# Optimization experiments

Measured on AMD Instinct MI355X. Metric: run time of the kernel, lower is better.

Reference implementation:

```python
import jax, jax.numpy as jnp
import numpy as np

N_NODES, N_EDGES, D = 50000, 640000, 128

def setup_inputs() -> dict:
    key = jax.random.key(0)
    ks = jax.random.split(key, 8)
    s = 0.05
    return {
        'node_h': jax.random.normal(ks[0], (N_NODES, D), jnp.float32),
        'edge_h': jax.random.normal(ks[1], (N_EDGES, D), jnp.float32),
        'src': jax.random.randint(ks[2], (N_EDGES,), 0, N_NODES, jnp.int32),
        'dst': jax.random.randint(ks[3], (N_EDGES,), 0, N_NODES, jnp.int32),
        'We1': jax.random.normal(ks[4], (3 * D, D), jnp.float32) * s,
        'be1': jnp.zeros((D,), jnp.float32),
        'We2': jax.random.normal(ks[5], (D, D), jnp.float32) * s,
        'be2': jnp.zeros((D,), jnp.float32),
        'Wn1': jax.random.normal(ks[6], (2 * D, D), jnp.float32) * s,
        'bn1': jnp.zeros((D,), jnp.float32),
        'Wn2': jax.random.normal(ks[7], (D, D), jnp.float32) * s,
        'bn2': jnp.zeros((D,), jnp.float32),
    }

def reference(node_h, edge_h, src, dst, We1, be1, We2, be2, Wn1, bn1, Wn2, bn2):
    # edge update: concat(src h, dst h, edge h) -> edge MLP  [E, 3D] -> [E, D]
    e_in = jnp.concatenate([node_h[src], node_h[dst], edge_h], axis=-1)
    e_new = jax.nn.relu(e_in @ We1 + be1) @ We2 + be2
    # message = copy_e('h'), reduce = sum -> segment_sum over destination nodes
    agg_m = jax.ops.segment_sum(e_new, dst, num_segments=node_h.shape[0])
    # node update: concat(agg_m, node h) -> node MLP  [N, 2D] -> [N, D]
    n_in = jnp.concatenate([agg_m, node_h], axis=-1)
    n_new = jax.nn.relu(n_in @ Wn1 + bn1) @ Wn2 + bn2
    return n_new
```

## Files before the change

### kernel.cpp

```cpp
#include <hip/hip_runtime.h>

#define NN 50000
#define NE 640000
#define DD 128

typedef float f32x4 __attribute__((ext_vector_type(4)));
typedef __bf16 bf16x8 __attribute__((ext_vector_type(8)));
typedef unsigned short u16x8 __attribute__((ext_vector_type(8)));

__device__ inline __bf16 f2bf(float f) {
  unsigned u = __builtin_bit_cast(unsigned, f);
  u = (u + 0x7fffu + ((u >> 16) & 1u)) >> 16;
  unsigned short h = (unsigned short)u;
  return __builtin_bit_cast(__bf16, h);
}
__device__ inline unsigned short f2bfu(float f) {
  return __builtin_bit_cast(unsigned short, f2bf(f));
}
__device__ inline float bf2f(unsigned bits16) {
  return __builtin_bit_cast(float, bits16 << 16);
}
__device__ inline float bfval(__bf16 h) {
  return bf2f((unsigned)__builtin_bit_cast(unsigned short, h));
}

__device__ inline bf16x8 load8(const float* __restrict__ p) {
  f32x4 a = *(const f32x4*)p;
  f32x4 b = *(const f32x4*)(p + 4);
  bf16x8 o;
  o[0] = f2bf(a[0]); o[1] = f2bf(a[1]); o[2] = f2bf(a[2]); o[3] = f2bf(a[3]);
  o[4] = f2bf(b[0]); o[5] = f2bf(b[1]); o[6] = f2bf(b[2]); o[7] = f2bf(b[3]);
  return o;
}

#define MFMA16(a, b, c) __builtin_amdgcn_mfma_f32_16x16x32_bf16((a), (b), (c), 0, 0, 0)

__global__ void prep_kernel(const float* __restrict__ We1, const float* __restrict__ We2,
                            const float* __restrict__ Wn1, const float* __restrict__ Wn2,
                            __bf16* __restrict__ We1t, __bf16* __restrict__ We2t,
                            __bf16* __restrict__ Wn1t, __bf16* __restrict__ Wn2t) {
  int i = blockIdx.x * blockDim.x + threadIdx.x;
  if (i < 49152) {
    int n = i / 384, k = i % 384;
    We1t[i] = f2bf(We1[k * 128 + n]);
  } else if (i < 65536) {
    int j = i - 49152; int n = j / 128, k = j % 128;
    We2t[j] = f2bf(We2[k * 128 + n]);
  } else if (i < 98304) {
    int j = i - 65536; int n = j / 256, k = j % 256;
    Wn1t[j] = f2bf(Wn1[k * 128 + n]);
  } else if (i < 114688) {
    int j = i - 98304; int n = j / 128, k = j % 128;
    Wn2t[j] = f2bf(Wn2[k * 128 + n]);
  }
}

__global__ void conv_node_kernel(const float* __restrict__ nh,
                                 unsigned short* __restrict__ nhb) {
  int i = blockIdx.x * 256 + threadIdx.x;
  if (i >= NN * DD / 8) return;
  const float* p = nh + (size_t)i * 8;
  f32x4 a = *(const f32x4*)p;
  f32x4 b = *(const f32x4*)(p + 4);
  u16x8 o;
  o[0] = f2bfu(a[0]); o[1] = f2bfu(a[1]); o[2] = f2bfu(a[2]); o[3] = f2bfu(a[3]);
  o[4] = f2bfu(b[0]); o[5] = f2bfu(b[1]); o[6] = f2bfu(b[2]); o[7] = f2bfu(b[3]);
  *(u16x8*)(nhb + (size_t)i * 8) = o;
}

__global__ void hist_kernel(const int* __restrict__ dst, int* __restrict__ counts) {
  int i = blockIdx.x * 256 + threadIdx.x;
  if (i < NE) atomicAdd(&counts[dst[i]], 1);
}
__global__ void scan1_kernel(const int* __restrict__ counts, int* __restrict__ basearr,
                             int* __restrict__ partials) {
  __shared__ int sd[256];
  int t = threadIdx.x;
  int i = blockIdx.x * 256 + t;
  int v = (i < NN) ? counts[i] : 0;
  sd[t] = v; __syncthreads();
  for (int off = 1; off < 256; off <<= 1) {
    int x = (t >= off) ? sd[t - off] : 0;
    __syncthreads();
    sd[t] += x;
    __syncthreads();
  }
  if (i < NN) basearr[i] = sd[t] - v;
  if (t == 255) partials[blockIdx.x] = sd[255];
}
__global__ void scan2_kernel(const int* __restrict__ partials, int* __restrict__ poff,
                             int nparts) {
  __shared__ int sd[256];
  int t = threadIdx.x;
  int v = (t < nparts) ? partials[t] : 0;
  sd[t] = v; __syncthreads();
  for (int off = 1; off < 256; off <<= 1) {
    int x = (t >= off) ? sd[t - off] : 0;
    __syncthreads();
    sd[t] += x;
    __syncthreads();
  }
  if (t < nparts) poff[t] = sd[t] - v;
}
__global__ void scan3_kernel(int* __restrict__ basearr, const int* __restrict__ poff) {
  int i = blockIdx.x * 256 + threadIdx.x;
  if (i < NN) basearr[i] += poff[blockIdx.x];
}
__global__ void scatter_kernel(const int* __restrict__ src, const int* __restrict__ dst,
                               const int* __restrict__ basearr, int* __restrict__ cursor,
                               int* __restrict__ eids, int* __restrict__ sidv,
                               int* __restrict__ dstv) {
  int i = blockIdx.x * 256 + threadIdx.x;
  if (i < NE) {
    int d = dst[i];
    int p = basearr[d] + atomicAdd(&cursor[d], 1);
    eids[p] = i;
    sidv[p] = src[i];
    dstv[p] = d;
  }
}

__global__ __launch_bounds__(256) void edge_agg_kernel(
    const unsigned short* __restrict__ nhb, const float* __restrict__ edge_h,
    const int* __restrict__ eids, const int* __restrict__ sidv,
    const int* __restrict__ dstv,
    const __bf16* __restrict__ We1t, const float* __restrict__ be1,
    float* __restrict__ S) {
  __shared__ unsigned short h1[128 * 136];
  __shared__ int dloc[128];
  const int tid = (int)threadIdx.x;
  const int w = tid >> 6;
  const int l = tid & 63;
  const int lm = l & 15;
  const int q = l >> 4;
  const int e0 = (int)blockIdx.x * 128;
  const int row0 = w * 32;

  if (tid < 128) dloc[tid] = dstv[e0 + tid];

  const int p0 = e0 + row0 + lm;
  const int p1 = p0 + 16;
  const unsigned short* gA0[2] = {nhb + (size_t)sidv[p0] * DD, nhb + (size_t)dstv[p0] * DD};
  const unsigned short* gA1[2] = {nhb + (size_t)sidv[p1] * DD, nhb + (size_t)dstv[p1] * DD};
  const float* eh0 = edge_h + (size_t)eids[p0] * DD;
  const float* eh1 = edge_h + (size_t)eids[p1] * DD;

  f32x4 acc[2][8];
#pragma unroll
  for (int nt = 0; nt < 8; ++nt) {
    float b = be1[nt * 16 + lm];
    acc[0][nt] = (f32x4){b, b, b, b};
    acc[1][nt] = (f32x4){b, b, b, b};
  }

#pragma unroll
  for (int step = 0; step < 8; ++step) {
    const int region = step >> 2;
    const int col = ((step & 3) * 32) + q * 8;
    bf16x8 a0 = __builtin_bit_cast(bf16x8, *(const u16x8*)(gA0[region] + col));
    bf16x8 a1 = __builtin_bit_cast(bf16x8, *(const u16x8*)(gA1[region] + col));
    const __bf16* bp = We1t + (size_t)lm * 384 + step * 32 + q * 8;
#pragma unroll
    for (int nt = 0; nt < 8; ++nt) {
      bf16x8 bb = *(const bf16x8*)(bp + nt * 16 * 384);
      acc[0][nt] = MFMA16(a0, bb, acc[0][nt]);
      acc[1][nt] = MFMA16(a1, bb, acc[1][nt]);
    }
  }
#pragma unroll
  for (int s2 = 0; s2 < 4; ++s2) {
    const int col = s2 * 32 + q * 8;
    bf16x8 a0 = load8(eh0 + col);
    bf16x8 a1 = load8(eh1 + col);
    const __bf16* bp = We1t + (size_t)lm * 384 + (8 + s2) * 32 + q * 8;
#pragma unroll
    for (int nt = 0; nt < 8; ++nt) {
      bf16x8 bb = *(const bf16x8*)(bp + nt * 16 * 384);
      acc[0][nt] = MFMA16(a0, bb, acc[0][nt]);
      acc[1][nt] = MFMA16(a1, bb, acc[1][nt]);
    }
  }

#pragma unroll
  for (int t = 0; t < 2; ++t)
#pragma unroll
    for (int nt = 0; nt < 8; ++nt)
#pragma unroll
      for (int r = 0; r < 4; ++r) {
        float v = acc[t][nt][r];
        v = v > 0.f ? v : 0.f;
        int m = row0 + t * 16 + q * 4 + r;
        h1[m * 136 + nt * 16 + lm] = f2bfu(v);
      }
  __syncthreads();

  {
    const int col = tid & 127;
    const int rbeg = (tid >> 7) * 64;
    const int rend = rbeg + 64;
    float a = 0.f;
    int dcur = dloc[rbeg];
    for (int r = rbeg; r < rend; ++r) {
      int d = dloc[r];
      if (d != dcur) {
        unsafeAtomicAdd(&S[(size_t)dcur * DD + col], a);
        a = 0.f;
        dcur = d;
      }
      a += bf2f((unsigned)h1[r * 136 + col]);
    }
    unsafeAtomicAdd(&S[(size_t)dcur * DD + col], a);
  }
}

__global__ __launch_bounds__(256) void node_kernel2(
    const unsigned short* __restrict__ nhb, const float* __restrict__ S,
    const int* __restrict__ counts,
    const __bf16* __restrict__ We2t, const float* __restrict__ be2,
    const __bf16* __restrict__ Wn1t, const float* __restrict__ bn1,
    const __bf16* __restrict__ Wn2t, const float* __restrict__ bn2,
    float* __restrict__ out) {
  __shared__ unsigned short h1[128 * 136];
  const int tid = (int)threadIdx.x;
  const int w = tid >> 6;
  const int l = tid & 63;
  const int lm = l & 15;
  const int q = l >> 4;
  const int n0 = (int)blockIdx.x * 128;
  const int row0 = w * 32;

  int r0 = n0 + row0 + lm;
  int r1 = r0 + 16;
  int c0 = r0 < NN ? r0 : NN - 1;
  int c1 = r1 < NN ? r1 : NN - 1;
  const float* s0p = S + (size_t)c0 * DD;
  const float* s1p = S + (size_t)c1 * DD;

  f32x4 acc[2][8];

  {
    float cnt0[4], cnt1[4];
#pragma unroll
    for (int r = 0; r < 4; ++r) {
      int ra = n0 + row0 + q * 4 + r;
      int rb = ra + 16;
      cnt0[r] = (ra < NN) ? (float)counts[ra] : 0.f;
      cnt1[r] = (rb < NN) ? (float)counts[rb] : 0.f;
    }
#pragma unroll
    for (int nt = 0; nt < 8; ++nt) {
      float b = be2[nt * 16 + lm];
#pragma unroll
      for (int r = 0; r < 4; ++r) {
        acc[0][nt][r] = cnt0[r] * b;
        acc[1][nt][r] = cnt1[r] * b;
      }
    }
  }
#pragma unroll
  for (int step = 0; step < 4; ++step) {
    const int col = step * 32 + q * 8;
    f32x4 x0a = *(const f32x4*)(s0p + col);
    f32x4 x0b = *(const f32x4*)(s0p + col + 4);
    f32x4 x1a = *(const f32x4*)(s1p + col);
    f32x4 x1b = *(const f32x4*)(s1p + col + 4);
    bf16x8 h0, l0, h8, l8;
#pragma unroll
    for (int j = 0; j < 4; ++j) {
      float v = x0a[j]; __bf16 hh = f2bf(v);
      h0[j] = hh; l0[j] = f2bf(v - bfval(hh));
      v = x0b[j]; hh = f2bf(v);
      h0[j + 4] = hh; l0[j + 4] = f2bf(v - bfval(hh));
      v = x1a[j]; hh = f2bf(v);
      h8[j] = hh; l8[j] = f2bf(v - bfval(hh));
      v = x1b[j]; hh = f2bf(v);
      h8[j + 4] = hh; l8[j + 4] = f2bf(v - bfval(hh));
    }
    const __bf16* bp = We2t + (size_t)lm * 128 + step * 32 + q * 8;
#pragma unroll
    for (int nt = 0; nt < 8; ++nt) {
      bf16x8 bb = *(const bf16x8*)(bp + nt * 16 * 128);
      acc[0][nt] = MFMA16(h0, bb, acc[0][nt]);
      acc[0][nt] = MFMA16(l0, bb, acc[0][nt]);
      acc[1][nt] = MFMA16(h8, bb, acc[1][nt]);
      acc[1][nt] = MFMA16(l8, bb, acc[1][nt]);
    }
  }

#pragma unroll
  for (int t = 0; t < 2; ++t)
#pragma unroll
    for (int nt = 0; nt < 8; ++nt)
#pragma unroll
      for (int r = 0; r < 4; ++r) {
        int m = row0 + t * 16 + q * 4 + r;
        h1[m * 136 + nt * 16 + lm] = f2bfu(acc[t][nt][r]);
      }
  __syncthreads();

#pragma unroll
  for (int nt = 0; nt < 8; ++nt) {
    float b = bn1[nt * 16 + lm];
    acc[0][nt] = (f32x4){b, b, b, b};
    acc[1][nt] = (f32x4){b, b, b, b};
  }
#pragma unroll
  for (int step = 0; step < 8; ++step) {
    bf16x8 a0, a1;
    if (step < 4) {
      a0 = __builtin_bit_cast(bf16x8, *(const u16x8*)&h1[(row0 + lm) * 136 + step * 32 + q * 8]);
      a1 = __builtin_bit_cast(bf16x8, *(const u16x8*)&h1[(row0 + 16 + lm) * 136 + step * 32 + q * 8]);
    } else {
      const int col = (step - 4) * 32 + q * 8;
      a0 = __builtin_bit_cast(bf16x8, *(const u16x8*)(nhb + (size_t)c0 * DD + col));
      a1 = __builtin_bit_cast(bf16x8, *(const u16x8*)(nhb + (size_t)c1 * DD + col));
    }
    const __bf16* bp = Wn1t + (size_t)lm * 256 + step * 32 + q * 8;
#pragma unroll
    for (int nt = 0; nt < 8; ++nt) {
      bf16x8 bb = *(const bf16x8*)(bp + nt * 16 * 256);
      acc[0][nt] = MFMA16(a0, bb, acc[0][nt]);
      acc[1][nt] = MFMA16(a1, bb, acc[1][nt]);
    }
  }
  __syncthreads();

#pragma unroll
  for (int t = 0; t < 2; ++t)
#pragma unroll
    for (int nt = 0; nt < 8; ++nt)
#pragma unroll
      for (int r = 0; r < 4; ++r) {
        float v = acc[t][nt][r];
        v = v > 0.f ? v : 0.f;
        int m = row0 + t * 16 + q * 4 + r;
        h1[m * 136 + nt * 16 + lm] = f2bfu(v);
      }
  __syncthreads();

#pragma unroll
  for (int nt = 0; nt < 8; ++nt) {
    float b = bn2[nt * 16 + lm];
    acc[0][nt] = (f32x4){b, b, b, b};
    acc[1][nt] = (f32x4){b, b, b, b};
  }
#pragma unroll
  for (int step = 0; step < 4; ++step) {
    bf16x8 a0 = __builtin_bit_cast(bf16x8, *(const u16x8*)&h1[(row0 + lm) * 136 + step * 32 + q * 8]);
    bf16x8 a1 = __builtin_bit_cast(bf16x8, *(const u16x8*)&h1[(row0 + 16 + lm) * 136 + step * 32 + q * 8]);
    const __bf16* bp = Wn2t + (size_t)lm * 128 + step * 32 + q * 8;
#pragma unroll
    for (int nt = 0; nt < 8; ++nt) {
      bf16x8 bb = *(const bf16x8*)(bp + nt * 16 * 128);
      acc[0][nt] = MFMA16(a0, bb, acc[0][nt]);
      acc[1][nt] = MFMA16(a1, bb, acc[1][nt]);
    }
  }

#pragma unroll
  for (int t = 0; t < 2; ++t) {
#pragma unroll
    for (int r = 0; r < 4; ++r) {
      int node = n0 + row0 + t * 16 + q * 4 + r;
      if (node < NN) {
        float* orow = out + (size_t)node * DD + lm;
#pragma unroll
        for (int nt = 0; nt < 8; ++nt)
          orow[nt * 16] = acc[t][nt][r];
      }
    }
  }
}

__global__ __launch_bounds__(256) void edge_fb_kernel(
    const float* __restrict__ node_h, const float* __restrict__ edge_h,
    const int* __restrict__ src, const int* __restrict__ dst,
    const __bf16* __restrict__ We1t, const float* __restrict__ be1,
    const __bf16* __restrict__ We2t, const float* __restrict__ be2,
    float* __restrict__ agg) {
  __shared__ unsigned short h1[128 * 136];
  const int tid = (int)threadIdx.x;
  const int w = tid >> 6;
  const int l = tid & 63;
  const int lm = l & 15;
  const int q = l >> 4;
  const int e0 = (int)blockIdx.x * 128;
  const int row0 = w * 32;

  const int eA0 = e0 + row0 + lm;
  const int eA1 = eA0 + 16;
  const float* srcA0[3];
  const float* srcA1[3];
  srcA0[0] = node_h + (size_t)src[eA0] * DD;
  srcA0[1] = node_h + (size_t)dst[eA0] * DD;
  srcA0[2] = edge_h + (size_t)eA0 * DD;
  srcA1[0] = node_h + (size_t)src[eA1] * DD;
  srcA1[1] = node_h + (size_t)dst[eA1] * DD;
  srcA1[2] = edge_h + (size_t)eA1 * DD;

  f32x4 acc[2][8];
#pragma unroll
  for (int nt = 0; nt < 8; ++nt) {
    float b = be1[nt * 16 + lm];
    acc[0][nt] = (f32x4){b, b, b, b};
    acc[1][nt] = (f32x4){b, b, b, b};
  }
#pragma unroll
  for (int step = 0; step < 12; ++step) {
    const int region = step >> 2;
    const int col = ((step & 3) * 32) + q * 8;
    bf16x8 a0 = load8(srcA0[region] + col);
    bf16x8 a1 = load8(srcA1[region] + col);
    const __bf16* bp = We1t + (size_t)lm * 384 + step * 32 + q * 8;
#pragma unroll
    for (int nt = 0; nt < 8; ++nt) {
      bf16x8 bb = *(const bf16x8*)(bp + nt * 16 * 384);
      acc[0][nt] = MFMA16(a0, bb, acc[0][nt]);
      acc[1][nt] = MFMA16(a1, bb, acc[1][nt]);
    }
  }
#pragma unroll
  for (int t = 0; t < 2; ++t)
#pragma unroll
    for (int nt = 0; nt < 8; ++nt)
#pragma unroll
      for (int r = 0; r < 4; ++r) {
        float v = acc[t][nt][r];
        v = v > 0.f ? v : 0.f;
        int m = row0 + t * 16 + q * 4 + r;
        h1[m * 136 + nt * 16 + lm] = f2bfu(v);
      }
  __syncthreads();
#pragma unroll
  for (int nt = 0; nt < 8; ++nt) {
    float b = be2[nt * 16 + lm];
    acc[0][nt] = (f32x4){b, b, b, b};
    acc[1][nt] = (f32x4){b, b, b, b};
  }
#pragma unroll
  for (int step = 0; step < 4; ++step) {
    bf16x8 a0 = __builtin_bit_cast(bf16x8, *(const u16x8*)&h1[(row0 + lm) * 136 + step * 32 + q * 8]);
    bf16x8 a1 = __builtin_bit_cast(bf16x8, *(const u16x8*)&h1[(row0 + 16 + lm) * 136 + step * 32 + q * 8]);
    const __bf16* bp = We2t + (size_t)lm * 128 + step * 32 + q * 8;
#pragma unroll
    for (int nt = 0; nt < 8; ++nt) {
      bf16x8 bb = *(const bf16x8*)(bp + nt * 16 * 128);
      acc[0][nt] = MFMA16(a0, bb, acc[0][nt]);
      acc[1][nt] = MFMA16(a1, bb, acc[1][nt]);
    }
  }
#pragma unroll
  for (int t = 0; t < 2; ++t) {
#pragma unroll
    for (int r = 0; r < 4; ++r) {
      int e = e0 + row0 + t * 16 + q * 4 + r;
      float* arow = agg + (size_t)dst[e] * DD + lm;
#pragma unroll
      for (int nt = 0; nt < 8; ++nt)
        unsafeAtomicAdd(arow + nt * 16, acc[t][nt][r]);
    }
  }
}

__global__ __launch_bounds__(256) void node_fb_kernel(
    const float* __restrict__ node_h, const float* __restrict__ agg,
    const __bf16* __restrict__ Wn1t, const float* __restrict__ bn1,
    const __bf16* __restrict__ Wn2t, const float* __restrict__ bn2,
    float* __restrict__ out) {
  __shared__ unsigned short h1[128 * 136];
  const int tid = (int)threadIdx.x;
  const int w = tid >> 6;
  const int l = tid & 63;
  const int lm = l & 15;
  const int q = l >> 4;
  const int n0 = (int)blockIdx.x * 128;
  const int row0 = w * 32;

  int r0 = n0 + row0 + lm;
  int r1 = r0 + 16;
  int c0 = r0 < NN ? r0 : NN - 1;
  int c1 = r1 < NN ? r1 : NN - 1;
  const float* srcA0[2] = {agg + (size_t)c0 * DD, node_h + (size_t)c0 * DD};
  const float* srcA1[2] = {agg + (size_t)c1 * DD, node_h + (size_t)c1 * DD};

  f32x4 acc[2][8];
#pragma unroll
  for (int nt = 0; nt < 8; ++nt) {
    float b = bn1[nt * 16 + lm];
    acc[0][nt] = (f32x4){b, b, b, b};
    acc[1][nt] = (f32x4){b, b, b, b};
  }
#pragma unroll
  for (int step = 0; step < 8; ++step) {
    const int region = step >> 2;
    const int col = ((step & 3) * 32) + q * 8;
    bf16x8 a0 = load8(srcA0[region] + col);
    bf16x8 a1 = load8(srcA1[region] + col);
    const __bf16* bp = Wn1t + (size_t)lm * 256 + step * 32 + q * 8;
#pragma unroll
    for (int nt = 0; nt < 8; ++nt) {
      bf16x8 bb = *(const bf16x8*)(bp + nt * 16 * 256);
      acc[0][nt] = MFMA16(a0, bb, acc[0][nt]);
      acc[1][nt] = MFMA16(a1, bb, acc[1][nt]);
    }
  }
#pragma unroll
  for (int t = 0; t < 2; ++t)
#pragma unroll
    for (int nt = 0; nt < 8; ++nt)
#pragma unroll
      for (int r = 0; r < 4; ++r) {
        float v = acc[t][nt][r];
        v = v > 0.f ? v : 0.f;
        int m = row0 + t * 16 + q * 4 + r;
        h1[m * 136 + nt * 16 + lm] = f2bfu(v);
      }
  __syncthreads();
#pragma unroll
  for (int nt = 0; nt < 8; ++nt) {
    float b = bn2[nt * 16 + lm];
    acc[0][nt] = (f32x4){b, b, b, b};
    acc[1][nt] = (f32x4){b, b, b, b};
  }
#pragma unroll
  for (int step = 0; step < 4; ++step) {
    bf16x8 a0 = __builtin_bit_cast(bf16x8, *(const u16x8*)&h1[(row0 + lm) * 136 + step * 32 + q * 8]);
    bf16x8 a1 = __builtin_bit_cast(bf16x8, *(const u16x8*)&h1[(row0 + 16 + lm) * 136 + step * 32 + q * 8]);
    const __bf16* bp = Wn2t + (size_t)lm * 128 + step * 32 + q * 8;
#pragma unroll
    for (int nt = 0; nt < 8; ++nt) {
      bf16x8 bb = *(const bf16x8*)(bp + nt * 16 * 128);
      acc[0][nt] = MFMA16(a0, bb, acc[0][nt]);
      acc[1][nt] = MFMA16(a1, bb, acc[1][nt]);
    }
  }
#pragma unroll
  for (int t = 0; t < 2; ++t) {
#pragma unroll
    for (int r = 0; r < 4; ++r) {
      int node = n0 + row0 + t * 16 + q * 4 + r;
      if (node < NN) {
        float* orow = out + (size_t)node * DD + lm;
#pragma unroll
        for (int nt = 0; nt < 8; ++nt)
          orow[nt * 16] = acc[t][nt][r];
      }
    }
  }
}

extern "C" void kernel_launch(void* const* d_in, const int* in_sizes, int n_in,
                              void* d_out, int out_size, void* d_ws, size_t ws_size,
                              hipStream_t stream) {
  const float* node_h = (const float*)d_in[0];
  const float* edge_h = (const float*)d_in[1];
  const int* src = (const int*)d_in[2];
  const int* dst = (const int*)d_in[3];
  const float* We1 = (const float*)d_in[4];
  const float* be1 = (const float*)d_in[5];
  const float* We2 = (const float*)d_in[6];
  const float* be2 = (const float*)d_in[7];
  const float* Wn1 = (const float*)d_in[8];
  const float* bn1 = (const float*)d_in[9];
  const float* Wn2 = (const float*)d_in[10];
  const float* bn2 = (const float*)d_in[11];

  const size_t o_S    = 0;
  const size_t o_nhb  = 25600000;
  const size_t o_we1  = 38400000;
  const size_t o_we2  = 38498304;
  const size_t o_wn1  = 38531072;
  const size_t o_wn2  = 38596608;
  const size_t o_cnt  = 38629376;
  const size_t o_base = 38829376;
  const size_t o_cur  = 39029376;
  const size_t o_poff = 39229376;
  const size_t o_eids = 39230400;
  const size_t o_sidv = 41790400;
  const size_t o_dstv = 44350400;
  const size_t csr_need = 46910400;

  char* ws = (char*)d_ws;

  if (ws_size >= csr_need) {
    float* S = (float*)(ws + o_S);
    unsigned short* nhb = (unsigned short*)(ws + o_nhb);
    __bf16* We1t = (__bf16*)(ws + o_we1);
    __bf16* We2t = (__bf16*)(ws + o_we2);
    __bf16* Wn1t = (__bf16*)(ws + o_wn1);
    __bf16* Wn2t = (__bf16*)(ws + o_wn2);
    int* counts  = (int*)(ws + o_cnt);
    int* basearr = (int*)(ws + o_base);
    int* cursor  = (int*)(ws + o_cur);
    int* poff    = (int*)(ws + o_poff);
    int* eids    = (int*)(ws + o_eids);
    int* sidv    = (int*)(ws + o_sidv);
    int* dstv    = (int*)(ws + o_dstv);

    hipMemsetAsync(S, 0, (size_t)NN * DD * sizeof(float), stream);
    hipMemsetAsync(counts, 0, NN * sizeof(int), stream);
    hipMemsetAsync(cursor, 0, NN * sizeof(int), stream);
    conv_node_kernel<<<(NN * DD / 8 + 255) / 256, 256, 0, stream>>>(node_h, nhb);
    prep_kernel<<<(114688 + 255) / 256, 256, 0, stream>>>(We1, We2, Wn1, Wn2,
                                                          We1t, We2t, Wn1t, Wn2t);
    hist_kernel<<<(NE + 255) / 256, 256, 0, stream>>>(dst, counts);
    const int nparts = (NN + 255) / 256;
    scan1_kernel<<<nparts, 256, 0, stream>>>(counts, basearr, cursor);
    scan2_kernel<<<1, 256, 0, stream>>>(cursor, poff, nparts);
    scan3_kernel<<<nparts, 256, 0, stream>>>(basearr, poff);
    hipMemsetAsync(cursor, 0, NN * sizeof(int), stream);
    scatter_kernel<<<(NE + 255) / 256, 256, 0, stream>>>(src, dst, basearr, cursor,
                                                         eids, sidv, dstv);
    edge_agg_kernel<<<NE / 128, 256, 0, stream>>>(nhb, edge_h, eids, sidv, dstv,
                                                  We1t, be1, S);
    node_kernel2<<<(NN + 127) / 128, 256, 0, stream>>>(nhb, S, counts,
                                                       We2t, be2, Wn1t, bn1,
                                                       Wn2t, bn2, (float*)d_out);
  } else {
    const size_t agg_bytes = (size_t)NN * DD * sizeof(float);
    float* agg = (float*)d_ws;
    char* wbase = ws + agg_bytes;
    __bf16* We1t = (__bf16*)(wbase);
    __bf16* We2t = (__bf16*)(wbase + 98304);
    __bf16* Wn1t = (__bf16*)(wbase + 98304 + 32768);
    __bf16* Wn2t = (__bf16*)(wbase + 98304 + 32768 + 65536);

    hipMemsetAsync(agg, 0, agg_bytes, stream);
    prep_kernel<<<(114688 + 255) / 256, 256, 0, stream>>>(We1, We2, Wn1, Wn2,
                                                          We1t, We2t, Wn1t, Wn2t);
    edge_fb_kernel<<<NE / 128, 256, 0, stream>>>(node_h, edge_h, src, dst,
                                                 We1t, be1, We2t, be2, agg);
    node_fb_kernel<<<(NN + 127) / 128, 256, 0, stream>>>(node_h, agg, Wn1t, bn1,
                                                         Wn2t, bn2, (float*)d_out);
  }
}
```

Measured before the change: 897.7 us.

## Precompute per-node dst projection of first edge layer and reuse per segment

Splits the first edge-MLP matmul so the destination-node third (plus bias) is computed once per node in a new kernel, instead of once per edge. The edge kernel now runs MFMAs only on the src and edge_h parts, then adds the precomputed per-destination vector. It stages that vector in LDS per distinct destination segment, with a global-memory fallback when a block has more than 64 segments. The change also prefetches operands into registers up front and folds scan3 into the scatter kernel. In exchange it adds a 25.6MB fp32 intermediate buffer, its write and reads, and extra synchronization in the edge kernel.

Measured after the change: 841.6 us. 1.07x faster.

```diff
diff --git a/kernel.cpp b/kernel.cpp
--- a/kernel.cpp
+++ b/kernel.cpp
@@ -68,6 +68,57 @@
   *(u16x8*)(nhb + (size_t)i * 8) = o;
 }
 
+__global__ __launch_bounds__(256) void dnode_kernel(
+    const unsigned short* __restrict__ nhb, const __bf16* __restrict__ We1t,
+    const float* __restrict__ be1, float* __restrict__ Dg) {
+  const int tid = (int)threadIdx.x;
+  const int w = tid >> 6;
+  const int l = tid & 63;
+  const int lm = l & 15;
+  const int q = l >> 4;
+  const int n0 = (int)blockIdx.x * 128;
+  const int row0 = w * 32;
+
+  int r0 = n0 + row0 + lm;
+  int r1 = r0 + 16;
+  int c0 = r0 < NN ? r0 : NN - 1;
+  int c1 = r1 < NN ? r1 : NN - 1;
+
+  f32x4 acc[2][8];
+#pragma unroll
+  for (int nt = 0; nt < 8; ++nt) {
+    float b = be1[nt * 16 + lm];
+    acc[0][nt] = (f32x4){b, b, b, b};
+    acc[1][nt] = (f32x4){b, b, b, b};
+  }
+#pragma unroll
+  for (int s = 0; s < 4; ++s) {
+    const int col = s * 32 + q * 8;
+    bf16x8 a0 = __builtin_bit_cast(bf16x8, *(const u16x8*)(nhb + (size_t)c0 * DD + col));
+    bf16x8 a1 = __builtin_bit_cast(bf16x8, *(const u16x8*)(nhb + (size_t)c1 * DD + col));
+    const __bf16* bp = We1t + (size_t)lm * 384 + 128 + s * 32 + q * 8;
+#pragma unroll
+    for (int nt = 0; nt < 8; ++nt) {
+      bf16x8 bb = *(const bf16x8*)(bp + nt * 16 * 384);
+      acc[0][nt] = MFMA16(a0, bb, acc[0][nt]);
+      acc[1][nt] = MFMA16(a1, bb, acc[1][nt]);
+    }
+  }
+#pragma unroll
+  for (int t = 0; t < 2; ++t) {
+#pragma unroll
+    for (int r = 0; r < 4; ++r) {
+      int node = n0 + row0 + t * 16 + q * 4 + r;
+      if (node < NN) {
+        float* orow = Dg + (size_t)node * DD + lm;
+#pragma unroll
+        for (int nt = 0; nt < 8; ++nt)
+          orow[nt * 16] = acc[t][nt][r];
+      }
+    }
+  }
+}
+
 __global__ void hist_kernel(const int* __restrict__ dst, int* __restrict__ counts) {
   int i = blockIdx.x * 256 + threadIdx.x;
   if (i < NE) atomicAdd(&counts[dst[i]], 1);
@@ -102,18 +153,14 @@
   }
   if (t < nparts) poff[t] = sd[t] - v;
 }
-__global__ void scan3_kernel(int* __restrict__ basearr, const int* __restrict__ poff) {
-  int i = blockIdx.x * 256 + threadIdx.x;
-  if (i < NN) basearr[i] += poff[blockIdx.x];
-}
 __global__ void scatter_kernel(const int* __restrict__ src, const int* __restrict__ dst,
-                               const int* __restrict__ basearr, int* __restrict__ cursor,
-                               int* __restrict__ eids, int* __restrict__ sidv,
-                               int* __restrict__ dstv) {
+                               const int* __restrict__ basearr, const int* __restrict__ poff,
+                               int* __restrict__ cursor, int* __restrict__ eids,
+                               int* __restrict__ sidv, int* __restrict__ dstv) {
   int i = blockIdx.x * 256 + threadIdx.x;
   if (i < NE) {
     int d = dst[i];
-    int p = basearr[d] + atomicAdd(&cursor[d], 1);
+    int p = basearr[d] + poff[d >> 8] + atomicAdd(&cursor[d], 1);
     eids[p] = i;
     sidv[p] = src[i];
     dstv[p] = d;
@@ -123,11 +170,15 @@
 __global__ __launch_bounds__(256) void edge_agg_kernel(
     const unsigned short* __restrict__ nhb, const float* __restrict__ edge_h,
     const int* __restrict__ eids, const int* __restrict__ sidv,
-    const int* __restrict__ dstv,
-    const __bf16* __restrict__ We1t, const float* __restrict__ be1,
-    float* __restrict__ S) {
+    const int* __restrict__ dstv, const float* __restrict__ Dg,
+    const __bf16* __restrict__ We1t, float* __restrict__ S) {
   __shared__ unsigned short h1[128 * 136];
   __shared__ int dloc[128];
+  __shared__ int sidx[128];
+  __shared__ int segdst[128];
+  __shared__ int wcnt0s, nsegS;
+  float* Dlds = (float*)h1;
+
   const int tid = (int)threadIdx.x;
   const int w = tid >> 6;
   const int l = tid & 63;
@@ -135,31 +186,77 @@
   const int q = l >> 4;
   const int e0 = (int)blockIdx.x * 128;
   const int row0 = w * 32;
-
-  if (tid < 128) dloc[tid] = dstv[e0 + tid];
-
   const int p0 = e0 + row0 + lm;
   const int p1 = p0 + 16;
-  const unsigned short* gA0[2] = {nhb + (size_t)sidv[p0] * DD, nhb + (size_t)dstv[p0] * DD};
-  const unsigned short* gA1[2] = {nhb + (size_t)sidv[p1] * DD, nhb + (size_t)dstv[p1] * DD};
-  const float* eh0 = edge_h + (size_t)eids[p0] * DD;
-  const float* eh1 = edge_h + (size_t)eids[p1] * DD;
+
+  const unsigned short* sp0 = nhb + (size_t)sidv[p0] * DD;
+  const unsigned short* sp1 = nhb + (size_t)sidv[p1] * DD;
+  const float* ehp0 = edge_h + (size_t)eids[p0] * DD;
+  const float* ehp1 = edge_h + (size_t)eids[p1] * DD;
+
+  u16x8 sa0[4], sa1[4];
+#pragma unroll
+  for (int s = 0; s < 4; ++s) {
+    sa0[s] = *(const u16x8*)(sp0 + s * 32 + q * 8);
+    sa1[s] = *(const u16x8*)(sp1 + s * 32 + q * 8);
+  }
+  bf16x8 ea0[4], ea1[4];
+#pragma unroll
+  for (int s = 0; s < 4; ++s) {
+    ea0[s] = load8(ehp0 + s * 32 + q * 8);
+    ea1[s] = load8(ehp1 + s * 32 + q * 8);
+  }
+
+  int d = 0, flag = 0, idx = 0;
+  if (tid < 128) {
+    d = dstv[e0 + tid];
+    dloc[tid] = d;
+    int dp = (tid == 0) ? -1 : dstv[e0 + tid - 1];
+    flag = (d != dp) ? 1 : 0;
+    unsigned long long mask = __ballot(flag);
+    int lane = tid & 63;
+    idx = (int)__popcll(mask & ((1ull << lane) - 1)) + flag - 1;
+    if (tid == 63) wcnt0s = (int)__popcll(mask);
+  }
+  __syncthreads();
+  if (tid < 128) {
+    if (tid >= 64) idx += wcnt0s;
+    sidx[tid] = idx;
+    if (flag) segdst[idx] = d;
+    if (tid == 127) nsegS = idx + 1;
+  }
+  __syncthreads();
+  const int nsegT = nsegS;
+
+  {
+    const int nstage = nsegT < 64 ? nsegT : 64;
+    const int total = nstage << 7;
+    for (int base = 0; base < total; base += 1024) {
+      float v[4];
+#pragma unroll
+      for (int u = 0; u < 4; ++u) {
+        int i = base + u * 256 + tid;
+        if (i < total) v[u] = Dg[(size_t)segdst[i >> 7] * DD + (i & 127)];
+      }
+#pragma unroll
+      for (int u = 0; u < 4; ++u) {
+        int i = base + u * 256 + tid;
+        if (i < total) Dlds[(i >> 7) * 129 + (i & 127)] = v[u];
+      }
+    }
+  }
 
   f32x4 acc[2][8];
 #pragma unroll
   for (int nt = 0; nt < 8; ++nt) {
-    float b = be1[nt * 16 + lm];
-    acc[0][nt] = (f32x4){b, b, b, b};
-    acc[1][nt] = (f32x4){b, b, b, b};
-  }
-
-#pragma unroll
-  for (int step = 0; step < 8; ++step) {
-    const int region = step >> 2;
-    const int col = ((step & 3) * 32) + q * 8;
-    bf16x8 a0 = __builtin_bit_cast(bf16x8, *(const u16x8*)(gA0[region] + col));
-    bf16x8 a1 = __builtin_bit_cast(bf16x8, *(const u16x8*)(gA1[region] + col));
-    const __bf16* bp = We1t + (size_t)lm * 384 + step * 32 + q * 8;
+    acc[0][nt] = (f32x4){0.f, 0.f, 0.f, 0.f};
+    acc[1][nt] = (f32x4){0.f, 0.f, 0.f, 0.f};
+  }
+#pragma unroll
+  for (int s = 0; s < 4; ++s) {
+    bf16x8 a0 = __builtin_bit_cast(bf16x8, sa0[s]);
+    bf16x8 a1 = __builtin_bit_cast(bf16x8, sa1[s]);
+    const __bf16* bp = We1t + (size_t)lm * 384 + s * 32 + q * 8;
 #pragma unroll
     for (int nt = 0; nt < 8; ++nt) {
       bf16x8 bb = *(const bf16x8*)(bp + nt * 16 * 384);
@@ -168,18 +265,45 @@
     }
   }
 #pragma unroll
-  for (int s2 = 0; s2 < 4; ++s2) {
-    const int col = s2 * 32 + q * 8;
-    bf16x8 a0 = load8(eh0 + col);
-    bf16x8 a1 = load8(eh1 + col);
-    const __bf16* bp = We1t + (size_t)lm * 384 + (8 + s2) * 32 + q * 8;
+  for (int s = 0; s < 4; ++s) {
+    const __bf16* bp = We1t + (size_t)lm * 384 + 256 + s * 32 + q * 8;
 #pragma unroll
     for (int nt = 0; nt < 8; ++nt) {
       bf16x8 bb = *(const bf16x8*)(bp + nt * 16 * 384);
-      acc[0][nt] = MFMA16(a0, bb, acc[0][nt]);
-      acc[1][nt] = MFMA16(a1, bb, acc[1][nt]);
-    }
-  }
+      acc[0][nt] = MFMA16(ea0[s], bb, acc[0][nt]);
+      acc[1][nt] = MFMA16(ea1[s], bb, acc[1][nt]);
+    }
+  }
+  __syncthreads();
+
+  if (nsegT <= 64) {
+#pragma unroll
+    for (int t = 0; t < 2; ++t)
+#pragma unroll
+      for (int r = 0; r < 4; ++r) {
+        int row = row0 + t * 16 + q * 4 + r;
+        int si = sidx[row];
+#pragma unroll
+        for (int nt = 0; nt < 8; ++nt) {
+          float v = acc[t][nt][r] + Dlds[si * 129 + nt * 16 + lm];
+          acc[t][nt][r] = v > 0.f ? v : 0.f;
+        }
+      }
+  } else {
+#pragma unroll
+    for (int t = 0; t < 2; ++t)
+#pragma unroll
+      for (int r = 0; r < 4; ++r) {
+        int row = row0 + t * 16 + q * 4 + r;
+        const float* drow = Dg + (size_t)dloc[row] * DD + lm;
+#pragma unroll
+        for (int nt = 0; nt < 8; ++nt) {
+          float v = acc[t][nt][r] + drow[nt * 16];
+          acc[t][nt][r] = v > 0.f ? v : 0.f;
+        }
+      }
+  }
+  __syncthreads();
 
 #pragma unroll
   for (int t = 0; t < 2; ++t)
@@ -187,10 +311,8 @@
     for (int nt = 0; nt < 8; ++nt)
 #pragma unroll
       for (int r = 0; r < 4; ++r) {
-        float v = acc[t][nt][r];
-        v = v > 0.f ? v : 0.f;
         int m = row0 + t * 16 + q * 4 + r;
-        h1[m * 136 + nt * 16 + lm] = f2bfu(v);
+        h1[m * 136 + nt * 16 + lm] = f2bfu(acc[t][nt][r]);
       }
   __syncthreads();
 
@@ -201,11 +323,11 @@
     float a = 0.f;
     int dcur = dloc[rbeg];
     for (int r = rbeg; r < rend; ++r) {
-      int d = dloc[r];
-      if (d != dcur) {
+      int dd = dloc[r];
+      if (dd != dcur) {
         unsafeAtomicAdd(&S[(size_t)dcur * DD + col], a);
         a = 0.f;
-        dcur = d;
+        dcur = dd;
       }
       a += bf2f((unsigned)h1[r * 136 + col]);
     }
@@ -566,24 +688,26 @@
   const float* bn2 = (const float*)d_in[11];
 
   const size_t o_S    = 0;
-  const size_t o_nhb  = 25600000;
-  const size_t o_we1  = 38400000;
-  const size_t o_we2  = 38498304;
-  const size_t o_wn1  = 38531072;
-  const size_t o_wn2  = 38596608;
-  const size_t o_cnt  = 38629376;
-  const size_t o_base = 38829376;
-  const size_t o_cur  = 39029376;
-  const size_t o_poff = 39229376;
-  const size_t o_eids = 39230400;
-  const size_t o_sidv = 41790400;
-  const size_t o_dstv = 44350400;
-  const size_t csr_need = 46910400;
+  const size_t o_D    = 25600000;
+  const size_t o_nhb  = 51200000;
+  const size_t o_we1  = 64000000;
+  const size_t o_we2  = 64098304;
+  const size_t o_wn1  = 64131072;
+  const size_t o_wn2  = 64196608;
+  const size_t o_cnt  = 64229376;
+  const size_t o_base = 64429376;
+  const size_t o_cur  = 64629376;
+  const size_t o_poff = 64829376;
+  const size_t o_eids = 64830400;
+  const size_t o_sidv = 67390400;
+  const size_t o_dstv = 69950400;
+  const size_t csr_need = 72510400;
 
   char* ws = (char*)d_ws;
 
   if (ws_size >= csr_need) {
-    float* S = (float*)(ws + o_S);
+    float* S     = (float*)(ws + o_S);
+    float* Dg    = (float*)(ws + o_D);
     unsigned short* nhb = (unsigned short*)(ws + o_nhb);
     __bf16* We1t = (__bf16*)(ws + o_we1);
     __bf16* We2t = (__bf16*)(ws + o_we2);
@@ -603,16 +727,16 @@
     conv_node_kernel<<<(NN * DD / 8 + 255) / 256, 256, 0, stream>>>(node_h, nhb);
     prep_kernel<<<(114688 + 255) / 256, 256, 0, stream>>>(We1, We2, Wn1, Wn2,
                                                           We1t, We2t, Wn1t, Wn2t);
+    dnode_kernel<<<(NN + 127) / 128, 256, 0, stream>>>(nhb, We1t, be1, Dg);
     hist_kernel<<<(NE + 255) / 256, 256, 0, stream>>>(dst, counts);
     const int nparts = (NN + 255) / 256;
     scan1_kernel<<<nparts, 256, 0, stream>>>(counts, basearr, cursor);
     scan2_kernel<<<1, 256, 0, stream>>>(cursor, poff, nparts);
-    scan3_kernel<<<nparts, 256, 0, stream>>>(basearr, poff);
     hipMemsetAsync(cursor, 0, NN * sizeof(int), stream);
-    scatter_kernel<<<(NE + 255) / 256, 256, 0, stream>>>(src, dst, basearr, cursor,
-                                                         eids, sidv, dstv);
+    scatter_kernel<<<(NE + 255) / 256, 256, 0, stream>>>(src, dst, basearr, poff,
+                                                         cursor, eids, sidv, dstv);
     edge_agg_kernel<<<NE / 128, 256, 0, stream>>>(nhb, edge_h, eids, sidv, dstv,
-                                                  We1t, be1, S);
+                                                  Dg, We1t, S);
     node_kernel2<<<(NN + 127) / 128, 256, 0, stream>>>(nhb, S, counts,
                                                        We2t, be2, Wn1t, bn1,
                                                        Wn2t, bn2, (float*)d_out);
```
